# Kernel tuning notes

Hardware: AMD Instinct MI355X
Metric: run time of the kernel (lower is better)

## Reference

```python
import jax, jax.numpy as jnp
import numpy as np

EPS = 1e-7

def fake_quant(x, bits):
    """Per-tensor affine fake-quantization (dnn-gating TorchRoundToBits),
    matching torch.fake_quantize_per_tensor_affine with dynamic range."""
    fp_max = jax.lax.stop_gradient(jnp.max(x))
    fp_min = jax.lax.stop_gradient(jnp.min(x))
    qmax = float(2 ** bits - 1)
    qmin = 0.0
    scale = (fp_max - fp_min) / (qmax - qmin) + EPS
    zero_point = jnp.trunc(qmin - fp_min / scale)  # int() cast in torch truncates
    q = jnp.round(x / scale + zero_point)
    qc = jnp.clip(q, qmin, qmax)
    return (qc - zero_point) * scale

def conv2d(x, w, stride=1, padding=1):
    return jax.lax.conv_general_dilated(
        x, w,
        window_strides=(stride, stride),
        padding=[(padding, padding), (padding, padding)],
        dimension_numbers=('NCHW', 'OIHW', 'NCHW'))

def setup_inputs() -> dict:
    key = jax.random.key(0)
    k1, k2 = jax.random.split(key)
    x = jax.random.normal(k1, (32, 256, 56, 56), dtype=jnp.float32)
    # kaiming-like init for a 3x3 conv with 256 in-channels
    fan_in = 256 * 3 * 3
    weight = jax.random.normal(k2, (256, 256, 3, 3), dtype=jnp.float32) / np.sqrt(fan_in)
    return {"x": x, "weight": weight}

def reference(x, weight):
    WBITS, ABITS, PGABITS = 8, 8, 4
    TH = 0.99
    w_q = fake_quant(weight, WBITS)          # quantized weights (shared by both convs)
    msb_in = fake_quant(x, PGABITS)          # low-precision (MSB) input
    msb_out = conv2d(msb_in, w_q)            # [32,256,56,56] prediction pass
    lsb_in = fake_quant(x, ABITS) - msb_in   # residual (LSB) input
    lsb_out = conv2d(lsb_in, w_q)            # high-precision correction pass
    mask = (jax.nn.sigmoid(msb_out) > TH).astype(msb_out.dtype)
    return msb_out + mask * lsb_out
```

## Files before the change

### kernel.cpp

```cpp
#include <hip/hip_runtime.h>
#include <stdint.h>
#include <stddef.h>

typedef int v4i  __attribute__((ext_vector_type(4)));
typedef int v16i __attribute__((ext_vector_type(16)));

struct QParams {
  float s4, z4, s8, z8, sw, zw;
  float s4sw, s8sw;
  int dw;
};

__device__ __forceinline__ unsigned enc_f(float f) {
  unsigned u = __float_as_uint(f);
  return (u & 0x80000000u) ? ~u : (u | 0x80000000u);
}
__device__ __forceinline__ float dec_f(unsigned e) {
  unsigned u = (e & 0x80000000u) ? (e ^ 0x80000000u) : ~e;
  return __uint_as_float(u);
}

__global__ void k_init(unsigned* mm, unsigned* zp) {
  int t = threadIdx.x;
  if (t < 128) zp[t] = 0u;
  if (t == 0) { mm[0] = 0xFFFFFFFFu; mm[1] = 0u; mm[2] = 0xFFFFFFFFu; mm[3] = 0u; }
}

__global__ void k_minmax(const float4* __restrict__ p, int n4, unsigned* mm) {
  float lmin = 3.4e38f, lmax = -3.4e38f;
  for (int i = blockIdx.x * blockDim.x + threadIdx.x; i < n4; i += gridDim.x * blockDim.x) {
    float4 v = p[i];
    lmin = fminf(lmin, fminf(fminf(v.x, v.y), fminf(v.z, v.w)));
    lmax = fmaxf(lmax, fmaxf(fmaxf(v.x, v.y), fmaxf(v.z, v.w)));
  }
  for (int off = 32; off; off >>= 1) {
    lmin = fminf(lmin, __shfl_down(lmin, off, 64));
    lmax = fmaxf(lmax, __shfl_down(lmax, off, 64));
  }
  __shared__ float smin[4], smax[4];
  int w = threadIdx.x >> 6, lane = threadIdx.x & 63;
  if (lane == 0) { smin[w] = lmin; smax[w] = lmax; }
  __syncthreads();
  if (threadIdx.x == 0) {
    float a = fminf(fminf(smin[0], smin[1]), fminf(smin[2], smin[3]));
    float b = fmaxf(fmaxf(smax[0], smax[1]), fmaxf(smax[2], smax[3]));
    atomicMin(&mm[0], enc_f(a));
    atomicMax(&mm[1], enc_f(b));
  }
}

__global__ void k_params(const unsigned* mm, QParams* q) {
  float xmin = dec_f(mm[0]), xmax = dec_f(mm[1]);
  float wmin = dec_f(mm[2]), wmax = dec_f(mm[3]);
  float s4 = (xmax - xmin) / 15.0f + 1e-7f;
  float z4 = truncf(0.0f - xmin / s4);
  float s8 = (xmax - xmin) / 255.0f + 1e-7f;
  float z8 = truncf(0.0f - xmin / s8);
  float sw = (wmax - wmin) / 255.0f + 1e-7f;
  float zw = truncf(0.0f - wmin / sw);
  q->s4 = s4; q->z4 = z4; q->s8 = s8; q->z8 = z8; q->sw = sw; q->zw = zw;
  q->s4sw = s4 * sw; q->s8sw = s8 * sw;
  q->dw = 128 - (int)zw;
}

__global__ void k_quant_w(const float* __restrict__ w, const QParams* __restrict__ q,
                          char* __restrict__ Wc) {
  __shared__ char sm[2304];
  int b = blockIdx.x;
  int tid = threadIdx.x;
  float sw = q->sw, zw = q->zw;
  const float* src = w + (size_t)b * 2304;
#pragma unroll
  for (int j = 0; j < 9; ++j) {
    int o = j * 256 + tid;
    float qf = rintf(__fdiv_rn(src[o], sw) + zw);
    qf = fminf(fmaxf(qf, 0.0f), 255.0f);
    int c = o / 9, jj = o - c * 9;
    sm[jj * 256 + c] = (char)((int)qf - 128);
  }
  __syncthreads();
  if (tid < 64) {
#pragma unroll
    for (int j = 0; j < 9; ++j)
      *(unsigned*)(Wc + (size_t)j * 65536 + b * 256 + tid * 4) =
          *(const unsigned*)(sm + j * 256 + tid * 4);
  }
}

__device__ __forceinline__ void quant2(float v, float s4, float z4, float s8, float z8,
                                       char& o4, char& o8) {
  float q4 = rintf(__fdiv_rn(v, s4) + z4);
  q4 = fminf(fmaxf(q4, 0.0f), 15.0f);
  o4 = (char)(int)(q4 - z4);
  float q8 = rintf(__fdiv_rn(v, s8) + z8);
  q8 = fminf(fmaxf(q8, 0.0f), 255.0f);
  int t8 = (int)(q8 - z8);
  o8 = (char)max(-128, min(127, t8));
}

__global__ void k_quant_x(const float4* __restrict__ x4, const QParams* __restrict__ q,
                          char* __restrict__ A4, char* __restrict__ A8,
                          int* __restrict__ CS4, int* __restrict__ CS8) {
  __shared__ char sm4[56 * 260];
  __shared__ char sm8[56 * 260];
  __shared__ int cp4[56][4], cp8[56][4];
  int bx = blockIdx.x;
  int n = bx / 56, y = bx % 56;
  int tid = threadIdx.x;
  float s4 = q->s4, z4 = q->z4, s8 = q->s8, z8 = q->z8;
  const float4* xrow = x4 + (size_t)n * 200704 + y * 14;
#pragma unroll 2
  for (int it = 0; it < 14; ++it) {
    int idx = it * 256 + tid;
    int c = idx / 14, xq = idx - c * 14;
    float4 v = xrow[(size_t)c * 784 + xq];
    int b = (xq * 4) * 260 + c;
    char a0, b0; quant2(v.x, s4, z4, s8, z8, a0, b0);
    char a1, b1; quant2(v.y, s4, z4, s8, z8, a1, b1);
    char a2, b2; quant2(v.z, s4, z4, s8, z8, a2, b2);
    char a3, b3; quant2(v.w, s4, z4, s8, z8, a3, b3);
    sm4[b] = a0; sm4[b + 260] = a1; sm4[b + 520] = a2; sm4[b + 780] = a3;
    sm8[b] = b0; sm8[b + 260] = b1; sm8[b + 520] = b2; sm8[b + 780] = b3;
  }
  __syncthreads();
  if (tid < 224) {
    int xc = tid >> 2, qq = tid & 3;
    const unsigned* r4 = (const unsigned*)(sm4 + xc * 260 + qq * 64);
    const unsigned* r8 = (const unsigned*)(sm8 + xc * 260 + qq * 64);
    int a = 0, b = 0;
#pragma unroll
    for (int cw = 0; cw < 16; ++cw) {
      unsigned u = r4[cw], v = r8[cw];
      a += (int)(signed char)(u) + (int)(signed char)(u >> 8)
         + (int)(signed char)(u >> 16) + (int)(signed char)(u >> 24);
      b += (int)(signed char)(v) + (int)(signed char)(v >> 8)
         + (int)(signed char)(v >> 16) + (int)(signed char)(v >> 24);
    }
    cp4[xc][qq] = a; cp8[xc][qq] = b;
  }
  __syncthreads();
  int pixbase = n * 3136 + y * 56;
  if (tid < 56) {
    CS4[pixbase + tid] = cp4[tid][0] + cp4[tid][1] + cp4[tid][2] + cp4[tid][3];
    CS8[pixbase + tid] = cp8[tid][0] + cp8[tid][1] + cp8[tid][2] + cp8[tid][3];
  }
  unsigned* A4w = (unsigned*)A4;
  unsigned* A8w = (unsigned*)A8;
#pragma unroll 2
  for (int it = 0; it < 14; ++it) {
    int idx = it * 256 + tid;
    int xc = idx >> 6, wd = idx & 63;
    size_t o = (size_t)(pixbase + xc) * 64 + wd;
    A4w[o] = *(const unsigned*)(sm4 + xc * 260 + wd * 4);
    A8w[o] = *(const unsigned*)(sm8 + xc * 260 + wd * 4);
  }
}

__global__ void k_wsum(const int* __restrict__ CS4, const int* __restrict__ CS8,
                       int* __restrict__ S4, int* __restrict__ S8) {
  int p = blockIdx.x * 256 + threadIdx.x;
  if (p >= 100352) return;
  int rem = p % 3136;
  int y = rem / 56, xc = rem % 56;
  int a = 0, b = 0;
#pragma unroll
  for (int dy = -1; dy <= 1; ++dy) {
    if ((unsigned)(y + dy) >= 56u) continue;
#pragma unroll
    for (int dx = -1; dx <= 1; ++dx) {
      if ((unsigned)(xc + dx) >= 56u) continue;
      int qq = p + dy * 56 + dx;
      a += CS4[qq]; b += CS8[qq];
    }
  }
  S4[p] = a; S8[p] = b;
}

#define GLD16(gp, lp)                                                         \
  __builtin_amdgcn_global_load_lds((const __attribute__((address_space(1))) void*)(gp), \
                                   (__attribute__((address_space(3))) void*)(lp), 16, 0, 0)

__device__ __forceinline__ float pg_merge(int a4v, int a8v, float fs4, float fs8) {
  float msb = fs4 * (float)a4v;
  float c8  = fs8 * (float)a8v;
  float lsb = c8 - msb;
  float sig = 1.0f / (1.0f + expf(-msb));
  return msb + (sig > 0.99f ? lsb : 0.0f);
}

struct StagePtrs {
  const char* aBase0; const char* aBase1;
  const char* a8Base0; const char* a8Base1;
  const char* bBase0; const char* bBase1;
  const char* zp0;
  unsigned vm0, vm1;
};

__device__ __forceinline__ void issue_stage(int s, const StagePtrs& P,
                                            char* dA4, char* dA8, char* dB) {
  int win = s >> 2;
  int cs = (s & 3) << 6;
  int dy = win / 3 - 1;
  int dx = win - (dy + 1) * 3 - 1;
  int doff = (dy * 56 + dx) * 256 + cs;
  bool ok0 = (P.vm0 >> win) & 1;
  bool ok1 = (P.vm1 >> win) & 1;
  const char* g40 = ok0 ? P.aBase0 + doff : P.zp0;
  const char* g41 = ok1 ? P.aBase1 + doff : P.zp0;
  const char* g80 = ok0 ? P.a8Base0 + doff : P.zp0;
  const char* g81 = ok1 ? P.a8Base1 + doff : P.zp0;
  const char* gB0 = P.bBase0 + win * 65536 + cs;
  const char* gB1 = P.bBase1 + win * 65536 + cs;
  if (s >= 36) { gB0 = P.zp0; gB1 = P.zp0; }
  GLD16(g40, dA4);       GLD16(g41, dA4 + 1024);
  GLD16(g80, dA8);       GLD16(g81, dA8 + 1024);
  GLD16(gB0, dB);        GLD16(gB1, dB + 1024);
}

__global__ __launch_bounds__(256, 2) void k_conv(
    const char* __restrict__ A4, const char* __restrict__ A8,
    const char* __restrict__ Wc,
    const int* __restrict__ S4, const int* __restrict__ S8,
    const QParams* __restrict__ q, const char* __restrict__ zpage,
    float* __restrict__ out) {
  __shared__ char smA4[3][8192], smA8[3][8192], smB[3][8192];
  const size_t ASZ = 25690112;
  int tid = threadIdx.x;
  int w = tid >> 6, lane = tid & 63;

  int bid = blockIdx.x;
  int swz = (bid & 7) * 196 + (bid >> 3);
  int m0 = (swz >> 1) * 128;
  int n0 = (swz & 1) * 128;
  int wm = w >> 1, wn = w & 1;

  int chunk = lane & 3;
  int r0 = (w << 5) + (lane >> 2);
  int r1 = r0 + 16;
  int cg0 = chunk ^ ((r0 >> 1) & 3);
  int cg1 = chunk ^ ((r1 >> 1) & 3);
  int p0 = m0 + r0, p1 = m0 + r1;
  int rem0 = p0 % 3136, rem1 = p1 % 3136;
  int y0 = rem0 / 56, x0 = rem0 % 56;
  int y1 = rem1 / 56, x1 = rem1 % 56;

  StagePtrs P;
  P.aBase0 = A4 + (size_t)p0 * 256 + cg0 * 16;
  P.aBase1 = A4 + (size_t)p1 * 256 + cg1 * 16;
  P.a8Base0 = P.aBase0 + ASZ;
  P.a8Base1 = P.aBase1 + ASZ;
  P.bBase0 = Wc + (n0 + r0) * 256 + cg0 * 16;
  P.bBase1 = Wc + (n0 + r1) * 256 + cg1 * 16;
  P.zp0 = zpage + chunk * 16;
  P.vm0 = 0; P.vm1 = 0;
#pragma unroll
  for (int win = 0; win < 9; ++win) {
    int dy = win / 3 - 1, dx = win % 3 - 1;
    P.vm0 |= (unsigned)(((unsigned)(y0 + dy) < 56u) & ((unsigned)(x0 + dx) < 56u)) << win;
    P.vm1 |= (unsigned)(((unsigned)(y1 + dy) < 56u) & ((unsigned)(x1 + dx) < 56u)) << win;
  }

  char* dA4 = &smA4[0][w << 11];
  char* dA8 = &smA8[0][w << 11];
  char* dB  = &smB[0][w << 11];
  const char* smA4f = &smA4[0][0];
  const char* smA8f = &smA8[0][0];
  const char* smBf  = &smB[0][0];

  v16i acc4[2][2] = {}, acc8[2][2] = {};
  int r31 = lane & 31, qh = lane >> 5;

  int offA[2][2], offB[2][2];
#pragma unroll
  for (int fm = 0; fm < 2; ++fm) {
    int row = wm * 64 + fm * 32 + r31;
    int swl = (row >> 1) & 3;
#pragma unroll
    for (int kc = 0; kc < 2; ++kc)
      offA[fm][kc] = row * 64 + (((kc * 2 + qh) ^ swl) << 4);
  }
#pragma unroll
  for (int fn = 0; fn < 2; ++fn) {
    int row = wn * 64 + fn * 32 + r31;
    int swl = (row >> 1) & 3;
#pragma unroll
    for (int kc = 0; kc < 2; ++kc)
      offB[fn][kc] = row * 64 + (((kc * 2 + qh) ^ swl) << 4);
  }

#define COMPUTE(BUF)                                                          \
  {                                                                           \
    _Pragma("unroll")                                                         \
    for (int kc = 0; kc < 2; ++kc) {                                          \
      v4i a4f[2], a8f[2], bf[2];                                              \
      _Pragma("unroll")                                                       \
      for (int fm = 0; fm < 2; ++fm) {                                        \
        a4f[fm] = *(const v4i*)(smA4f + (BUF) * 8192 + offA[fm][kc]);         \
        a8f[fm] = *(const v4i*)(smA8f + (BUF) * 8192 + offA[fm][kc]);         \
      }                                                                       \
      _Pragma("unroll")                                                       \
      for (int fn = 0; fn < 2; ++fn)                                          \
        bf[fn] = *(const v4i*)(smBf + (BUF) * 8192 + offB[fn][kc]);           \
      _Pragma("unroll")                                                       \
      for (int fm = 0; fm < 2; ++fm)                                          \
        _Pragma("unroll")                                                     \
        for (int fn = 0; fn < 2; ++fn) {                                      \
          acc4[fm][fn] = __builtin_amdgcn_mfma_i32_32x32x32_i8(a4f[fm], bf[fn], acc4[fm][fn], 0, 0, 0); \
          acc8[fm][fn] = __builtin_amdgcn_mfma_i32_32x32x32_i8(a8f[fm], bf[fn], acc8[fm][fn], 0, 0, 0); \
        }                                                                     \
    }                                                                         \
  }

  issue_stage(0, P, dA4, dA8, dB);
  issue_stage(1, P, dA4 + 8192, dA8 + 8192, dB + 8192);

#define PHASE(S, RB, WB)                                                      \
  {                                                                           \
    asm volatile("s_waitcnt vmcnt(6)" ::: "memory");                          \
    asm volatile("s_barrier" ::: "memory");                                   \
    issue_stage((S) + 2, P, dA4 + (WB) * 8192, dA8 + (WB) * 8192,             \
                dB + (WB) * 8192);                                            \
    __builtin_amdgcn_s_setprio(1);                                            \
    COMPUTE(RB);                                                              \
    __builtin_amdgcn_s_setprio(0);                                            \
  }

#pragma unroll 1
  for (int sp = 0; sp < 12; ++sp) {
    int s0 = sp * 3;
    PHASE(s0,     0, 2);
    PHASE(s0 + 1, 1, 0);
    PHASE(s0 + 2, 2, 1);
  }
  asm volatile("s_waitcnt vmcnt(0)" ::: "memory");
#undef PHASE
#undef COMPUTE

  float fs4 = q->s4sw, fs8 = q->s8sw;
  int dwv = q->dw;
#pragma unroll
  for (int fm = 0; fm < 2; ++fm)
#pragma unroll
    for (int fn = 0; fn < 2; ++fn) {
      int kout = n0 + wn * 64 + fn * 32 + r31;
      int pb = m0 + wm * 64 + fm * 32 + 4 * qh;
#pragma unroll
      for (int rg = 0; rg < 4; ++rg) {
        int pr = pb + 8 * rg;
        int4 sv4 = *(const int4*)(S4 + pr);
        int4 sv8 = *(const int4*)(S8 + pr);
        float4 res;
        res.x = pg_merge(acc4[fm][fn][rg * 4 + 0] + dwv * sv4.x,
                         acc8[fm][fn][rg * 4 + 0] + dwv * sv8.x, fs4, fs8);
        res.y = pg_merge(acc4[fm][fn][rg * 4 + 1] + dwv * sv4.y,
                         acc8[fm][fn][rg * 4 + 1] + dwv * sv8.y, fs4, fs8);
        res.z = pg_merge(acc4[fm][fn][rg * 4 + 2] + dwv * sv4.z,
                         acc8[fm][fn][rg * 4 + 2] + dwv * sv8.z, fs4, fs8);
        res.w = pg_merge(acc4[fm][fn][rg * 4 + 3] + dwv * sv4.w,
                         acc8[fm][fn][rg * 4 + 3] + dwv * sv8.w, fs4, fs8);
        int nimg = pr / 3136;
        int rem = pr - nimg * 3136;
        *(float4*)(out + (size_t)nimg * 802816 + (size_t)kout * 3136 + rem) = res;
      }
    }
}

extern "C" void kernel_launch(void* const* d_in, const int* in_sizes, int n_in,
                              void* d_out, int out_size, void* d_ws, size_t ws_size,
                              hipStream_t stream) {
  const float* x  = (const float*)d_in[0];
  const float* wt = (const float*)d_in[1];
  float* out = (float*)d_out;

  char* ws = (char*)d_ws;
  unsigned* mm = (unsigned*)ws;
  QParams* prm = (QParams*)(ws + 64);
  char* zpage = ws + 256;
  char* A4 = ws + 1024;
  const size_t ASZ = 25690112;
  char* A8 = A4 + ASZ;
  int* CS4 = (int*)(A8 + ASZ);
  int* CS8 = CS4 + 100352;
  int* S4  = CS8 + 100352;
  int* S8  = S4 + 100352;
  char* Wc = (char*)(S8 + 100352);

  k_init<<<1, 256, 0, stream>>>(mm, (unsigned*)zpage);
  k_minmax<<<1024, 256, 0, stream>>>((const float4*)x, 25690112 / 4, mm);
  k_minmax<<<64, 256, 0, stream>>>((const float4*)wt, 589824 / 4, mm + 2);
  k_params<<<1, 1, 0, stream>>>(mm, prm);
  k_quant_w<<<256, 256, 0, stream>>>(wt, prm, Wc);
  k_quant_x<<<1792, 256, 0, stream>>>((const float4*)x, prm, A4, A8, CS4, CS8);
  k_wsum<<<392, 256, 0, stream>>>(CS4, CS8, S4, S8);
  k_conv<<<dim3(1568), 256, 0, stream>>>(A4, A8, Wc, S4, S8, prm, zpage, out);
}
```

Before: 422.5 us.

## Split conv stage loads into halves interleaved with MFMA subphases; merge minmax launches

The conv main loop is restructured so each stage's global-to-LDS loads are issued in two halves, one per k-chunk subphase. Each subphase first reads its fragments from LDS, then issues the next half load, syncs, and runs its MFMAs, so load issue is spread across the compute instead of sitting in one burst. The x and weight min/max reductions are also merged into a single launch to save one kernel launch. The extra barriers and lgkmcnt waits per subphase add synchronisation cost, and the ordering of LDS reads against buffer overwrites depends on the new barrier placement.

```diff
diff --git a/kernel.cpp b/kernel.cpp
--- a/kernel.cpp
+++ b/kernel.cpp
@@ -26,9 +26,13 @@
   if (t == 0) { mm[0] = 0xFFFFFFFFu; mm[1] = 0u; mm[2] = 0xFFFFFFFFu; mm[3] = 0u; }
 }
 
-__global__ void k_minmax(const float4* __restrict__ p, int n4, unsigned* mm) {
+__global__ void k_minmax2(const float4* __restrict__ x, int nx4,
+                          const float4* __restrict__ w, int nw4, unsigned* mm) {
+  const float4* p; int n4; unsigned* slot; int base; int nblk;
+  if (blockIdx.x < 1024) { p = x; n4 = nx4; slot = mm;     base = blockIdx.x;        nblk = 1024; }
+  else                   { p = w; n4 = nw4; slot = mm + 2; base = blockIdx.x - 1024; nblk = 64; }
   float lmin = 3.4e38f, lmax = -3.4e38f;
-  for (int i = blockIdx.x * blockDim.x + threadIdx.x; i < n4; i += gridDim.x * blockDim.x) {
+  for (int i = base * blockDim.x + threadIdx.x; i < n4; i += nblk * blockDim.x) {
     float4 v = p[i];
     lmin = fminf(lmin, fminf(fminf(v.x, v.y), fminf(v.z, v.w)));
     lmax = fmaxf(lmax, fmaxf(fmaxf(v.x, v.y), fmaxf(v.z, v.w)));
@@ -38,14 +42,14 @@
     lmax = fmaxf(lmax, __shfl_down(lmax, off, 64));
   }
   __shared__ float smin[4], smax[4];
-  int w = threadIdx.x >> 6, lane = threadIdx.x & 63;
-  if (lane == 0) { smin[w] = lmin; smax[w] = lmax; }
+  int w2 = threadIdx.x >> 6, lane = threadIdx.x & 63;
+  if (lane == 0) { smin[w2] = lmin; smax[w2] = lmax; }
   __syncthreads();
   if (threadIdx.x == 0) {
     float a = fminf(fminf(smin[0], smin[1]), fminf(smin[2], smin[3]));
     float b = fmaxf(fmaxf(smax[0], smax[1]), fmaxf(smax[2], smax[3]));
-    atomicMin(&mm[0], enc_f(a));
-    atomicMax(&mm[1], enc_f(b));
+    atomicMin(&slot[0], enc_f(a));
+    atomicMax(&slot[1], enc_f(b));
   }
 }
 
@@ -196,8 +200,8 @@
   unsigned vm0, vm1;
 };
 
-__device__ __forceinline__ void issue_stage(int s, const StagePtrs& P,
-                                            char* dA4, char* dA8, char* dB) {
+__device__ __forceinline__ void issue_half(int s, int half, const StagePtrs& P,
+                                           char* dA4, char* dA8, char* dB) {
   int win = s >> 2;
   int cs = (s & 3) << 6;
   int dy = win / 3 - 1;
@@ -205,16 +209,19 @@
   int doff = (dy * 56 + dx) * 256 + cs;
   bool ok0 = (P.vm0 >> win) & 1;
   bool ok1 = (P.vm1 >> win) & 1;
-  const char* g40 = ok0 ? P.aBase0 + doff : P.zp0;
-  const char* g41 = ok1 ? P.aBase1 + doff : P.zp0;
-  const char* g80 = ok0 ? P.a8Base0 + doff : P.zp0;
-  const char* g81 = ok1 ? P.a8Base1 + doff : P.zp0;
-  const char* gB0 = P.bBase0 + win * 65536 + cs;
-  const char* gB1 = P.bBase1 + win * 65536 + cs;
-  if (s >= 36) { gB0 = P.zp0; gB1 = P.zp0; }
-  GLD16(g40, dA4);       GLD16(g41, dA4 + 1024);
-  GLD16(g80, dA8);       GLD16(g81, dA8 + 1024);
-  GLD16(gB0, dB);        GLD16(gB1, dB + 1024);
+  if (half == 0) {
+    const char* g40 = ok0 ? P.aBase0 + doff : P.zp0;
+    const char* g41 = ok1 ? P.aBase1 + doff : P.zp0;
+    const char* gB0 = P.bBase0 + win * 65536 + cs;
+    if (s >= 36) gB0 = P.zp0;
+    GLD16(g40, dA4); GLD16(g41, dA4 + 1024); GLD16(gB0, dB);
+  } else {
+    const char* g80 = ok0 ? P.a8Base0 + doff : P.zp0;
+    const char* g81 = ok1 ? P.a8Base1 + doff : P.zp0;
+    const char* gB1 = P.bBase1 + win * 65536 + cs;
+    if (s >= 36) gB1 = P.zp0;
+    GLD16(g80, dA8); GLD16(g81, dA8 + 1024); GLD16(gB1, dB + 1024);
+  }
 }
 
 __global__ __launch_bounds__(256, 2) void k_conv(
@@ -288,42 +295,44 @@
       offB[fn][kc] = row * 64 + (((kc * 2 + qh) ^ swl) << 4);
   }
 
-#define COMPUTE(BUF)                                                          \
+#define SUBPHASE(S, RB, WB, KC)                                               \
   {                                                                           \
+    v4i a4f[2], a8f[2], bf[2];                                                \
     _Pragma("unroll")                                                         \
-    for (int kc = 0; kc < 2; ++kc) {                                          \
-      v4i a4f[2], a8f[2], bf[2];                                              \
+    for (int fm = 0; fm < 2; ++fm) {                                          \
+      a4f[fm] = *(const v4i*)(smA4f + (RB) * 8192 + offA[fm][KC]);            \
+      a8f[fm] = *(const v4i*)(smA8f + (RB) * 8192 + offA[fm][KC]);            \
+    }                                                                         \
+    _Pragma("unroll")                                                         \
+    for (int fn = 0; fn < 2; ++fn)                                            \
+      bf[fn] = *(const v4i*)(smBf + (RB) * 8192 + offB[fn][KC]);              \
+    issue_half((S) + 2, KC, P, dA4 + (WB) * 8192, dA8 + (WB) * 8192,          \
+               dB + (WB) * 8192);                                             \
+    asm volatile("s_barrier" ::: "memory");                                   \
+    asm volatile("s_waitcnt lgkmcnt(0)" ::: "memory");                        \
+    __builtin_amdgcn_s_setprio(1);                                            \
+    _Pragma("unroll")                                                         \
+    for (int fm = 0; fm < 2; ++fm)                                            \
       _Pragma("unroll")                                                       \
-      for (int fm = 0; fm < 2; ++fm) {                                        \
-        a4f[fm] = *(const v4i*)(smA4f + (BUF) * 8192 + offA[fm][kc]);         \
-        a8f[fm] = *(const v4i*)(smA8f + (BUF) * 8192 + offA[fm][kc]);         \
+      for (int fn = 0; fn < 2; ++fn) {                                        \
+        acc4[fm][fn] = __builtin_amdgcn_mfma_i32_32x32x32_i8(a4f[fm], bf[fn], acc4[fm][fn], 0, 0, 0); \
+        acc8[fm][fn] = __builtin_amdgcn_mfma_i32_32x32x32_i8(a8f[fm], bf[fn], acc8[fm][fn], 0, 0, 0); \
       }                                                                       \
-      _Pragma("unroll")                                                       \
-      for (int fn = 0; fn < 2; ++fn)                                          \
-        bf[fn] = *(const v4i*)(smBf + (BUF) * 8192 + offB[fn][kc]);           \
-      _Pragma("unroll")                                                       \
-      for (int fm = 0; fm < 2; ++fm)                                          \
-        _Pragma("unroll")                                                     \
-        for (int fn = 0; fn < 2; ++fn) {                                      \
-          acc4[fm][fn] = __builtin_amdgcn_mfma_i32_32x32x32_i8(a4f[fm], bf[fn], acc4[fm][fn], 0, 0, 0); \
-          acc8[fm][fn] = __builtin_amdgcn_mfma_i32_32x32x32_i8(a8f[fm], bf[fn], acc8[fm][fn], 0, 0, 0); \
-        }                                                                     \
-    }                                                                         \
-  }
-
-  issue_stage(0, P, dA4, dA8, dB);
-  issue_stage(1, P, dA4 + 8192, dA8 + 8192, dB + 8192);
+    __builtin_amdgcn_s_setprio(0);                                            \
+  }
 
 #define PHASE(S, RB, WB)                                                      \
   {                                                                           \
     asm volatile("s_waitcnt vmcnt(6)" ::: "memory");                          \
     asm volatile("s_barrier" ::: "memory");                                   \
-    issue_stage((S) + 2, P, dA4 + (WB) * 8192, dA8 + (WB) * 8192,             \
-                dB + (WB) * 8192);                                            \
-    __builtin_amdgcn_s_setprio(1);                                            \
-    COMPUTE(RB);                                                              \
-    __builtin_amdgcn_s_setprio(0);                                            \
-  }
+    SUBPHASE(S, RB, WB, 0)                                                    \
+    SUBPHASE(S, RB, WB, 1)                                                    \
+  }
+
+  issue_half(0, 0, P, dA4, dA8, dB);
+  issue_half(0, 1, P, dA4, dA8, dB);
+  issue_half(1, 0, P, dA4 + 8192, dA8 + 8192, dB + 8192);
+  issue_half(1, 1, P, dA4 + 8192, dA8 + 8192, dB + 8192);
 
 #pragma unroll 1
   for (int sp = 0; sp < 12; ++sp) {
@@ -334,7 +343,7 @@
   }
   asm volatile("s_waitcnt vmcnt(0)" ::: "memory");
 #undef PHASE
-#undef COMPUTE
+#undef SUBPHASE
 
   float fs4 = q->s4sw, fs8 = q->s8sw;
   int dwv = q->dw;
@@ -386,8 +395,8 @@
   char* Wc = (char*)(S8 + 100352);
 
   k_init<<<1, 256, 0, stream>>>(mm, (unsigned*)zpage);
-  k_minmax<<<1024, 256, 0, stream>>>((const float4*)x, 25690112 / 4, mm);
-  k_minmax<<<64, 256, 0, stream>>>((const float4*)wt, 589824 / 4, mm + 2);
+  k_minmax2<<<1088, 256, 0, stream>>>((const float4*)x, 25690112 / 4,
+                                      (const float4*)wt, 589824 / 4, mm);
   k_params<<<1, 1, 0, stream>>>(mm, prm);
   k_quant_w<<<256, 256, 0, stream>>>(wt, prm, Wc);
   k_quant_x<<<1792, 256, 0, stream>>>((const float4*)x, prm, A4, A8, CS4, CS8);
```

New measurement: 408.4 us. 1.03x faster.
